# Performance work log

Hardware: AMD Instinct MI355X
Metric: run time of the kernel (lower is better)

The kernel has to match this reference:

```python
import jax, jax.numpy as jnp
import numpy as np

N_NODES = 50000
N_EDGES = 400000
N_GRAPHS = 64
DN = 64    # node features
DE = 64    # edge features
DG = 16    # global features
DH = 128   # mlp hidden
DO = 64    # mlp output
NHID = 2   # hidden layers
E_IN = 2 * DN + DE + DG   # 208
N_IN = DN + DO + DG       # 144


def _mlp_params(key, d_in, d_h, d_out, n_hid):
    ks = jax.random.split(key, 3)
    w_in = jax.random.normal(ks[0], (d_in, d_h), jnp.float32) * (2.0 / d_in) ** 0.5
    w_h = jax.random.normal(ks[1], (n_hid, d_h, d_h), jnp.float32) * (2.0 / d_h) ** 0.5
    w_out = jax.random.normal(ks[2], (d_h, d_out), jnp.float32) * (2.0 / d_h) ** 0.5
    return (w_in, jnp.zeros((d_h,), jnp.float32), w_h, jnp.zeros((n_hid, d_h), jnp.float32),
            w_out, jnp.zeros((d_out,), jnp.float32), jnp.ones((d_out,), jnp.float32),
            jnp.zeros((d_out,), jnp.float32))


def _mlp(h, w_in, b_in, w_h, b_h, w_out, b_out, g, b):
    # Lin -> [relu, Lin]*NHID -> relu -> Lin -> LayerNorm  (dropout=0 at eval)
    h = h @ w_in + b_in
    for i in range(w_h.shape[0]):
        h = jax.nn.relu(h) @ w_h[i] + b_h[i]
    h = jax.nn.relu(h) @ w_out + b_out
    mu = jnp.mean(h, axis=-1, keepdims=True)
    var = jnp.mean((h - mu) ** 2, axis=-1, keepdims=True)
    return (h - mu) * jax.lax.rsqrt(var + 1e-5) * g + b


def setup_inputs() -> dict:
    key = jax.random.key(0)
    k = jax.random.split(key, 8)
    x = jax.random.normal(k[0], (N_NODES, DN), jnp.float32)
    edge_attr = jax.random.normal(k[1], (N_EDGES, DE), jnp.float32)
    u = jax.random.normal(k[2], (N_GRAPHS, DG), jnp.float32)
    edge_index = jax.random.randint(k[3], (2, N_EDGES), 0, N_NODES, dtype=jnp.int32)
    batch = jnp.sort(jax.random.randint(k[4], (N_NODES,), 0, N_GRAPHS, dtype=jnp.int32))
    names = ["w_in", "b_in", "w_h", "b_h", "w_out", "b_out", "ln_g", "ln_b"]
    d = {"x": x, "edge_attr": edge_attr, "u": u, "edge_index": edge_index, "batch": batch}
    for pref, kk, d_in in (("e_", k[5], E_IN), ("a_", k[6], E_IN), ("n_", k[7], N_IN)):
        for nm, v in zip(names, _mlp_params(kk, d_in, DH, DO, NHID)):
            d[pref + nm] = v
    return d


def reference(x, edge_attr, u, edge_index, batch,
              e_w_in, e_b_in, e_w_h, e_b_h, e_w_out, e_b_out, e_ln_g, e_ln_b,
              a_w_in, a_b_in, a_w_h, a_b_h, a_w_out, a_b_out, a_ln_g, a_ln_b,
              n_w_in, n_b_in, n_w_h, n_b_h, n_w_out, n_b_out, n_ln_g, n_ln_b):
    src, tgt = edge_index[0], edge_index[1]
    edge_batch = batch[src]
    # EdgeModel: gather src/tgt node feats + global feats, concat, MLP (+ sigmoid attention MLP)
    neigh = jnp.concatenate([x[src], x[tgt], edge_attr, u[edge_batch]], axis=1)  # [E, E_IN]
    e_out = _mlp(neigh, e_w_in, e_b_in, e_w_h, e_b_h, e_w_out, e_b_out, e_ln_g, e_ln_b)
    attn = jax.nn.sigmoid(_mlp(neigh, a_w_in, a_b_in, a_w_h, a_b_h, a_w_out, a_b_out, a_ln_g, a_ln_b))
    e_out = e_out * attn  # [E, DO]
    # NodeModel: scatter-sum incoming (target-indexed) edge outputs, concat, MLP
    agg = jax.ops.segment_sum(e_out, tgt, num_segments=x.shape[0])  # [N, DO], zeros for isolated nodes
    node_in = jnp.concatenate([x, agg, u[batch]], axis=1)  # [N, N_IN]
    x_out = _mlp(node_in, n_w_in, n_b_in, n_w_h, n_b_h, n_w_out, n_b_out, n_ln_g, n_ln_b)
    return x_out
```

## Files before the change

kernel.cpp:

```cpp
#include <hip/hip_runtime.h>
#include <math.h>

#define N_NODES 50000
#define N_EDGES 400000

typedef _Float16 half8 __attribute__((ext_vector_type(8)));
typedef float f32x4 __attribute__((ext_vector_type(4)));

#define LD1 232
#define LDH 136
#define LDN 168

#define AGG_OFF 0
#define XH_OFF  12800000
#define UH_OFF  19200000
#define WP_OFF  19202048
#define O_EW1 0
#define O_EH0 28672
#define O_EH1 45056
#define O_EWO 61440
#define O_AW1 69632
#define O_AH0 98304
#define O_AH1 114688
#define O_AWO 131072
#define O_NW1 139264
#define O_NH0 159744
#define O_NH1 176128
#define O_NWO 192512

__device__ __forceinline__ f32x4 mfma16(half8 a, half8 b, f32x4 c) {
  return __builtin_amdgcn_mfma_f32_16x16x32_f16(a, b, c, 0, 0, 0);
}

__device__ __forceinline__ void gemm_h(const _Float16* __restrict__ src,
                                       _Float16* __restrict__ dst,
                                       const _Float16* __restrict__ wp16,
                                       const float* __restrict__ bias,
                                       int w, int lane) {
  const half8* wp = (const half8*)wp16;
  const int r = lane & 15, ch = lane >> 4;
  f32x4 a0[4], a1[4];
#pragma unroll
  for (int m = 0; m < 4; ++m) {
    a0[m] = (f32x4){0.f, 0.f, 0.f, 0.f};
    a1[m] = (f32x4){0.f, 0.f, 0.f, 0.f};
  }
#pragma unroll
  for (int s = 0; s < 4; ++s) {
    half8 b0 = wp[(s * 4 + ch) * 128 + w * 32 + r];
    half8 b1 = wp[(s * 4 + ch) * 128 + w * 32 + 16 + r];
#pragma unroll
    for (int m = 0; m < 4; ++m) {
      half8 a = *(const half8*)(src + (m * 16 + r) * LDH + s * 32 + ch * 8);
      a0[m] = mfma16(a, b0, a0[m]);
      a1[m] = mfma16(a, b1, a1[m]);
    }
  }
  float bb0 = bias[w * 32 + r], bb1 = bias[w * 32 + 16 + r];
#pragma unroll
  for (int m = 0; m < 4; ++m)
#pragma unroll
    for (int q = 0; q < 4; ++q) {
      int row = m * 16 + ch * 4 + q;
      dst[row * LDH + w * 32 + r]      = (_Float16)fmaxf(a0[m][q] + bb0, 0.f);
      dst[row * LDH + w * 32 + 16 + r] = (_Float16)fmaxf(a1[m][q] + bb1, 0.f);
    }
}

__device__ __forceinline__ void gemm_l1_dual(const _Float16* __restrict__ sIn,
                                             _Float16* __restrict__ dQ,
                                             _Float16* __restrict__ dR,
                                             const _Float16* wpE16, const _Float16* wpA16,
                                             const float* __restrict__ bE,
                                             const float* __restrict__ bA,
                                             int w, int lane) {
  const half8* wpE = (const half8*)wpE16;
  const half8* wpA = (const half8*)wpA16;
  const int r = lane & 15, ch = lane >> 4;
  f32x4 e0[4], e1[4], q0[4], q1[4];
#pragma unroll
  for (int m = 0; m < 4; ++m) {
    e0[m] = (f32x4){0.f, 0.f, 0.f, 0.f}; e1[m] = (f32x4){0.f, 0.f, 0.f, 0.f};
    q0[m] = (f32x4){0.f, 0.f, 0.f, 0.f}; q1[m] = (f32x4){0.f, 0.f, 0.f, 0.f};
  }
#pragma unroll
  for (int s = 0; s < 7; ++s) {
    half8 be0 = wpE[(s * 4 + ch) * 128 + w * 32 + r];
    half8 be1 = wpE[(s * 4 + ch) * 128 + w * 32 + 16 + r];
    half8 ba0 = wpA[(s * 4 + ch) * 128 + w * 32 + r];
    half8 ba1 = wpA[(s * 4 + ch) * 128 + w * 32 + 16 + r];
#pragma unroll
    for (int m = 0; m < 4; ++m) {
      half8 a = *(const half8*)(sIn + (m * 16 + r) * LD1 + s * 32 + ch * 8);
      e0[m] = mfma16(a, be0, e0[m]);
      e1[m] = mfma16(a, be1, e1[m]);
      q0[m] = mfma16(a, ba0, q0[m]);
      q1[m] = mfma16(a, ba1, q1[m]);
    }
  }
  float be0v = bE[w * 32 + r], be1v = bE[w * 32 + 16 + r];
  float ba0v = bA[w * 32 + r], ba1v = bA[w * 32 + 16 + r];
#pragma unroll
  for (int m = 0; m < 4; ++m)
#pragma unroll
    for (int q = 0; q < 4; ++q) {
      int row = m * 16 + ch * 4 + q;
      dQ[row * LDH + w * 32 + r]      = (_Float16)fmaxf(e0[m][q] + be0v, 0.f);
      dQ[row * LDH + w * 32 + 16 + r] = (_Float16)fmaxf(e1[m][q] + be1v, 0.f);
      dR[row * LDH + w * 32 + r]      = (_Float16)fmaxf(q0[m][q] + ba0v, 0.f);
      dR[row * LDH + w * 32 + 16 + r] = (_Float16)fmaxf(q1[m][q] + ba1v, 0.f);
    }
}

__device__ __forceinline__ void gemm_l1n(const _Float16* __restrict__ sIn,
                                         _Float16* __restrict__ dst,
                                         const _Float16* wp16,
                                         const float* __restrict__ bias,
                                         int w, int lane) {
  const half8* wp = (const half8*)wp16;
  const int r = lane & 15, ch = lane >> 4;
  f32x4 a0[4], a1[4];
#pragma unroll
  for (int m = 0; m < 4; ++m) {
    a0[m] = (f32x4){0.f, 0.f, 0.f, 0.f};
    a1[m] = (f32x4){0.f, 0.f, 0.f, 0.f};
  }
#pragma unroll
  for (int s = 0; s < 5; ++s) {
    half8 b0 = wp[(s * 4 + ch) * 128 + w * 32 + r];
    half8 b1 = wp[(s * 4 + ch) * 128 + w * 32 + 16 + r];
#pragma unroll
    for (int m = 0; m < 4; ++m) {
      half8 a = *(const half8*)(sIn + (m * 16 + r) * LDN + s * 32 + ch * 8);
      a0[m] = mfma16(a, b0, a0[m]);
      a1[m] = mfma16(a, b1, a1[m]);
    }
  }
  float bb0 = bias[w * 32 + r], bb1 = bias[w * 32 + 16 + r];
#pragma unroll
  for (int m = 0; m < 4; ++m)
#pragma unroll
    for (int q = 0; q < 4; ++q) {
      int row = m * 16 + ch * 4 + q;
      dst[row * LDH + w * 32 + r]      = (_Float16)fmaxf(a0[m][q] + bb0, 0.f);
      dst[row * LDH + w * 32 + 16 + r] = (_Float16)fmaxf(a1[m][q] + bb1, 0.f);
    }
}

struct EdgeP {
  const float* edge_attr; const int* edge_index; const int* batch;
  const _Float16* x_h; const _Float16* u_h; const _Float16* wp;
  const float *eBin, *eBh, *eBout, *eG, *eBt;
  const float *aBin, *aBh, *aBout, *aG, *aBt;
  float* agg;
};

__global__ __launch_bounds__(256, 2) void edge_kernel(EdgeP p) {
  __shared__ __align__(16) _Float16 sIn[64 * LD1];
  __shared__ __align__(16) _Float16 sQ[64 * LDH];
  __shared__ __align__(16) _Float16 sR[64 * LDH];
  __shared__ int sSrc[64], sTgt[64], sEb[64];
  const int tid = threadIdx.x;
  const int e0 = blockIdx.x * 64;

  if (tid < 64) {
    int s = p.edge_index[e0 + tid];
    sSrc[tid] = s;
    sTgt[tid] = p.edge_index[N_EDGES + e0 + tid];
    sEb[tid] = p.batch[s];
  }
  __syncthreads();

  for (int idx = tid; idx < 64 * 32; idx += 256) {
    int c = idx & 31, e = idx >> 5;
    if (c >= 29) continue;
    int col = c * 8;
    half8 v;
    if (col < 64) {
      v = *(const half8*)(p.x_h + (size_t)sSrc[e] * 64 + col);
    } else if (col < 128) {
      v = *(const half8*)(p.x_h + (size_t)sTgt[e] * 64 + col - 64);
    } else if (col < 192) {
      const float* ea = p.edge_attr + (size_t)(e0 + e) * 64 + (col - 128);
      float4 f0 = *(const float4*)ea, f1 = *(const float4*)(ea + 4);
      v[0] = (_Float16)f0.x; v[1] = (_Float16)f0.y;
      v[2] = (_Float16)f0.z; v[3] = (_Float16)f0.w;
      v[4] = (_Float16)f1.x; v[5] = (_Float16)f1.y;
      v[6] = (_Float16)f1.z; v[7] = (_Float16)f1.w;
    } else if (col < 208) {
      v = *(const half8*)(p.u_h + sEb[e] * 16 + col - 192);
    } else {
#pragma unroll
      for (int j = 0; j < 8; ++j) v[j] = (_Float16)0.f;
    }
    *(half8*)(sIn + e * LD1 + col) = v;
  }
  __syncthreads();

  const int lane = tid & 63, w = tid >> 6;
  _Float16* sP = sIn;

  gemm_l1_dual(sIn, sQ, sR, p.wp + O_EW1, p.wp + O_AW1, p.eBin, p.aBin, w, lane);
  __syncthreads();
  gemm_h(sQ, sP, p.wp + O_EH0, p.eBh, w, lane);        __syncthreads();
  gemm_h(sR, sQ, p.wp + O_AH0, p.aBh, w, lane);        __syncthreads();
  gemm_h(sP, sR, p.wp + O_EH1, p.eBh + 128, w, lane);  __syncthreads();
  gemm_h(sQ, sP, p.wp + O_AH1, p.aBh + 128, w, lane);  __syncthreads();

  const int r = lane & 15, ch = lane >> 4;
  const half8* wpEo = (const half8*)(p.wp + O_EWO);
  const half8* wpAo = (const half8*)(p.wp + O_AWO);
  f32x4 accE[4], accA[4];
#pragma unroll
  for (int t = 0; t < 4; ++t) {
    accE[t] = (f32x4){0.f, 0.f, 0.f, 0.f};
    accA[t] = (f32x4){0.f, 0.f, 0.f, 0.f};
  }
#pragma unroll
  for (int s = 0; s < 4; ++s) {
    half8 hE = *(const half8*)(sR + (w * 16 + r) * LDH + s * 32 + ch * 8);
    half8 hA = *(const half8*)(sP + (w * 16 + r) * LDH + s * 32 + ch * 8);
#pragma unroll
    for (int t = 0; t < 4; ++t) {
      half8 bEf = wpEo[(s * 4 + ch) * 64 + t * 16 + r];
      half8 bAf = wpAo[(s * 4 + ch) * 64 + t * 16 + r];
      accE[t] = mfma16(hE, bEf, accE[t]);
      accA[t] = mfma16(hA, bAf, accA[t]);
    }
  }
  float gE[4], tE[4], gA[4], tA[4];
#pragma unroll
  for (int t = 0; t < 4; ++t) {
    int cidx = t * 16 + r;
    float boE = p.eBout[cidx], boA = p.aBout[cidx];
#pragma unroll
    for (int q = 0; q < 4; ++q) { accE[t][q] += boE; accA[t][q] += boA; }
    gE[t] = p.eG[cidx]; tE[t] = p.eBt[cidx];
    gA[t] = p.aG[cidx]; tA[t] = p.aBt[cidx];
  }
#pragma unroll
  for (int q = 0; q < 4; ++q) {
    float s1e = 0.f, s2e = 0.f, s1a = 0.f, s2a = 0.f;
#pragma unroll
    for (int t = 0; t < 4; ++t) {
      float v = accE[t][q]; s1e += v; s2e += v * v;
      float u = accA[t][q]; s1a += u; s2a += u * u;
    }
#pragma unroll
    for (int mk = 1; mk < 16; mk <<= 1) {
      s1e += __shfl_xor(s1e, mk); s2e += __shfl_xor(s2e, mk);
      s1a += __shfl_xor(s1a, mk); s2a += __shfl_xor(s2a, mk);
    }
    float mue = s1e * (1.f / 64), mua = s1a * (1.f / 64);
    float rse = rsqrtf(s2e * (1.f / 64) - mue * mue + 1e-5f);
    float rsa = rsqrtf(s2a * (1.f / 64) - mua * mua + 1e-5f);
    int row = w * 16 + ch * 4 + q;
    float* ap = p.agg + (size_t)sTgt[row] * 64 + r;
#pragma unroll
    for (int t = 0; t < 4; ++t) {
      float oe = (accE[t][q] - mue) * rse * gE[t] + tE[t];
      float oa = (accA[t][q] - mua) * rsa * gA[t] + tA[t];
      atomicAdd(ap + t * 16, oe / (1.f + __expf(-oa)));
    }
  }
}

struct NodeP {
  const float* agg; const _Float16* x_h; const _Float16* u_h;
  const _Float16* wp; const int* batch;
  const float *Bin, *Bh, *Bout, *G, *Bt;
  float* out;
};

__global__ __launch_bounds__(256, 2) void node_kernel(NodeP p) {
  __shared__ __align__(16) _Float16 sIn[64 * LDN];
  __shared__ __align__(16) _Float16 sQ[64 * LDH];
  __shared__ int sB[64];
  const int tid = threadIdx.x;
  const int n0 = blockIdx.x * 64;

  if (tid < 64) {
    int n = n0 + tid;
    sB[tid] = (n < N_NODES) ? p.batch[n] : 0;
  }
  __syncthreads();

  for (int idx = tid; idx < 64 * 32; idx += 256) {
    int c = idx & 31, e = idx >> 5;
    if (c >= 21) continue;
    int n = n0 + e, col = c * 8;
    half8 v;
    if (n >= N_NODES || col >= 144) {
#pragma unroll
      for (int j = 0; j < 8; ++j) v[j] = (_Float16)0.f;
    } else if (col < 64) {
      v = *(const half8*)(p.x_h + (size_t)n * 64 + col);
    } else if (col < 128) {
      const float* ag = p.agg + (size_t)n * 64 + (col - 64);
      float4 f0 = *(const float4*)ag, f1 = *(const float4*)(ag + 4);
      v[0] = (_Float16)f0.x; v[1] = (_Float16)f0.y;
      v[2] = (_Float16)f0.z; v[3] = (_Float16)f0.w;
      v[4] = (_Float16)f1.x; v[5] = (_Float16)f1.y;
      v[6] = (_Float16)f1.z; v[7] = (_Float16)f1.w;
    } else {
      v = *(const half8*)(p.u_h + sB[e] * 16 + col - 128);
    }
    *(half8*)(sIn + e * LDN + col) = v;
  }
  __syncthreads();

  const int lane = tid & 63, w = tid >> 6;
  _Float16* sP = sIn;

  gemm_l1n(sIn, sQ, p.wp + O_NW1, p.Bin, w, lane);      __syncthreads();
  gemm_h(sQ, sP, p.wp + O_NH0, p.Bh, w, lane);          __syncthreads();
  gemm_h(sP, sQ, p.wp + O_NH1, p.Bh + 128, w, lane);    __syncthreads();

  const int r = lane & 15, ch = lane >> 4;
  const half8* wpNo = (const half8*)(p.wp + O_NWO);
  f32x4 acc[4];
#pragma unroll
  for (int t = 0; t < 4; ++t) acc[t] = (f32x4){0.f, 0.f, 0.f, 0.f};
#pragma unroll
  for (int s = 0; s < 4; ++s) {
    half8 h = *(const half8*)(sQ + (w * 16 + r) * LDH + s * 32 + ch * 8);
#pragma unroll
    for (int t = 0; t < 4; ++t) {
      half8 b = wpNo[(s * 4 + ch) * 64 + t * 16 + r];
      acc[t] = mfma16(h, b, acc[t]);
    }
  }
  float g[4], bt[4];
#pragma unroll
  for (int t = 0; t < 4; ++t) {
    int cidx = t * 16 + r;
    float bo = p.Bout[cidx];
#pragma unroll
    for (int q = 0; q < 4; ++q) acc[t][q] += bo;
    g[t] = p.G[cidx]; bt[t] = p.Bt[cidx];
  }
#pragma unroll
  for (int q = 0; q < 4; ++q) {
    float s1 = 0.f, s2 = 0.f;
#pragma unroll
    for (int t = 0; t < 4; ++t) { float v = acc[t][q]; s1 += v; s2 += v * v; }
#pragma unroll
    for (int mk = 1; mk < 16; mk <<= 1) {
      s1 += __shfl_xor(s1, mk); s2 += __shfl_xor(s2, mk);
    }
    float mu = s1 * (1.f / 64);
    float rs = rsqrtf(s2 * (1.f / 64) - mu * mu + 1e-5f);
    int row = w * 16 + ch * 4 + q;
    int n = n0 + row;
    if (n < N_NODES) {
#pragma unroll
      for (int t = 0; t < 4; ++t)
        p.out[(size_t)n * 64 + t * 16 + r] = (acc[t][q] - mu) * rs * g[t] + bt[t];
    }
  }
}

#define GX 112
struct PackP {
  const float* src[12];
  int Kreal[12], Nlog[12], size[12], dstoff[12];
  const float* x; const float* u;
  _Float16* x_h; _Float16* u_h; _Float16* wdst;
};

__global__ void pack_kernel(PackP p) {
  int y = blockIdx.y;
  int idx = blockIdx.x * 256 + threadIdx.x;
  if (y < 12) {
    int sz = p.size[y];
    if (idx >= sz) return;
    int N = 1 << p.Nlog[y];
    int j = idx & 7, t = idx >> 3;
    int n = t & (N - 1);
    int sc = t >> p.Nlog[y];
    int c = sc & 3, s = sc >> 2;
    int k = s * 32 + c * 8 + j;
    p.wdst[p.dstoff[y] + idx] =
        (k < p.Kreal[y]) ? (_Float16)p.src[y][k * N + n] : (_Float16)0.f;
  } else {
    for (int i = idx; i < N_NODES * 64; i += GX * 256) p.x_h[i] = (_Float16)p.x[i];
    for (int i = idx; i < 64 * 16; i += GX * 256) p.u_h[i] = (_Float16)p.u[i];
  }
}

extern "C" void kernel_launch(void* const* d_in, const int* in_sizes, int n_in,
                              void* d_out, int out_size, void* d_ws, size_t ws_size,
                              hipStream_t stream) {
  const float* x = (const float*)d_in[0];
  const float* edge_attr = (const float*)d_in[1];
  const float* u = (const float*)d_in[2];
  const int* edge_index = (const int*)d_in[3];
  const int* batch = (const int*)d_in[4];

  char* ws = (char*)d_ws;
  float* agg = (float*)(ws + AGG_OFF);
  _Float16* x_h = (_Float16*)(ws + XH_OFF);
  _Float16* u_h = (_Float16*)(ws + UH_OFF);
  _Float16* wp = (_Float16*)(ws + WP_OFF);

  hipMemsetAsync(agg, 0, (size_t)N_NODES * 64 * sizeof(float), stream);

  PackP pk;
  const float* eWh = (const float*)d_in[7];
  const float* aWh = (const float*)d_in[15];
  const float* nWh = (const float*)d_in[23];
  const float* srcs[12] = {
      (const float*)d_in[5], eWh, eWh + 16384, (const float*)d_in[9],
      (const float*)d_in[13], aWh, aWh + 16384, (const float*)d_in[17],
      (const float*)d_in[21], nWh, nWh + 16384, (const float*)d_in[25]};
  const int kr[12] = {208, 128, 128, 128, 208, 128, 128, 128, 144, 128, 128, 128};
  const int nl[12] = {7, 7, 7, 6, 7, 7, 7, 6, 7, 7, 7, 6};
  const int sz[12] = {28672, 16384, 16384, 8192, 28672, 16384, 16384, 8192,
                      20480, 16384, 16384, 8192};
  const int off[12] = {O_EW1, O_EH0, O_EH1, O_EWO, O_AW1, O_AH0, O_AH1, O_AWO,
                       O_NW1, O_NH0, O_NH1, O_NWO};
  for (int i = 0; i < 12; ++i) {
    pk.src[i] = srcs[i]; pk.Kreal[i] = kr[i]; pk.Nlog[i] = nl[i];
    pk.size[i] = sz[i]; pk.dstoff[i] = off[i];
  }
  pk.x = x; pk.u = u; pk.x_h = x_h; pk.u_h = u_h; pk.wdst = wp;
  pack_kernel<<<dim3(GX, 13), 256, 0, stream>>>(pk);

  EdgeP ep;
  ep.edge_attr = edge_attr; ep.edge_index = edge_index; ep.batch = batch;
  ep.x_h = x_h; ep.u_h = u_h; ep.wp = wp;
  ep.eBin = (const float*)d_in[6];  ep.eBh = (const float*)d_in[8];
  ep.eBout = (const float*)d_in[10]; ep.eG = (const float*)d_in[11];
  ep.eBt = (const float*)d_in[12];
  ep.aBin = (const float*)d_in[14]; ep.aBh = (const float*)d_in[16];
  ep.aBout = (const float*)d_in[18]; ep.aG = (const float*)d_in[19];
  ep.aBt = (const float*)d_in[20];
  ep.agg = agg;
  edge_kernel<<<N_EDGES / 64, 256, 0, stream>>>(ep);

  NodeP np;
  np.agg = agg; np.x_h = x_h; np.u_h = u_h; np.wp = wp; np.batch = batch;
  np.Bin = (const float*)d_in[22]; np.Bh = (const float*)d_in[24];
  np.Bout = (const float*)d_in[26]; np.G = (const float*)d_in[27];
  np.Bt = (const float*)d_in[28];
  np.out = (float*)d_out;
  node_kernel<<<(N_NODES + 63) / 64, 256, 0, stream>>>(np);
}
```

Baseline: 594.4 us.

## Split edge and attention MLPs across separate wave groups in 512-thread blocks

The edge kernel now runs 512 threads: waves 0-3 compute the edge MLP and waves 4-7 compute the attention MLP concurrently, each with its own ping-pong LDS buffers, instead of four waves computing both MLPs serially. The attention waves write sigmoid values to shared memory and the edge waves combine them before the scatter-add atomics. Index staging in shared memory is removed; each thread reads edge_index and batch directly, and the zero-padding column of the input tile is no longer written. This halves the per-wave serial GEMM chain and raises parallelism, at the cost of more LDS per block (four buffers) and an extra barrier; launch bounds of 512 threads with 4 blocks per CU may restrict registers.

```diff
diff --git a/kernel.cpp b/kernel.cpp
--- a/kernel.cpp
+++ b/kernel.cpp
@@ -32,7 +32,8 @@
   return __builtin_amdgcn_mfma_f32_16x16x32_f16(a, b, c, 0, 0, 0);
 }
 
-__device__ __forceinline__ void gemm_h(const _Float16* __restrict__ src,
+template<int NS, int LDSRC>
+__device__ __forceinline__ void gemm32(const _Float16* __restrict__ src,
                                        _Float16* __restrict__ dst,
                                        const _Float16* __restrict__ wp16,
                                        const float* __restrict__ bias,
@@ -46,92 +47,12 @@
     a1[m] = (f32x4){0.f, 0.f, 0.f, 0.f};
   }
 #pragma unroll
-  for (int s = 0; s < 4; ++s) {
+  for (int s = 0; s < NS; ++s) {
     half8 b0 = wp[(s * 4 + ch) * 128 + w * 32 + r];
     half8 b1 = wp[(s * 4 + ch) * 128 + w * 32 + 16 + r];
 #pragma unroll
     for (int m = 0; m < 4; ++m) {
-      half8 a = *(const half8*)(src + (m * 16 + r) * LDH + s * 32 + ch * 8);
-      a0[m] = mfma16(a, b0, a0[m]);
-      a1[m] = mfma16(a, b1, a1[m]);
-    }
-  }
-  float bb0 = bias[w * 32 + r], bb1 = bias[w * 32 + 16 + r];
-#pragma unroll
-  for (int m = 0; m < 4; ++m)
-#pragma unroll
-    for (int q = 0; q < 4; ++q) {
-      int row = m * 16 + ch * 4 + q;
-      dst[row * LDH + w * 32 + r]      = (_Float16)fmaxf(a0[m][q] + bb0, 0.f);
-      dst[row * LDH + w * 32 + 16 + r] = (_Float16)fmaxf(a1[m][q] + bb1, 0.f);
-    }
-}
-
-__device__ __forceinline__ void gemm_l1_dual(const _Float16* __restrict__ sIn,
-                                             _Float16* __restrict__ dQ,
-                                             _Float16* __restrict__ dR,
-                                             const _Float16* wpE16, const _Float16* wpA16,
-                                             const float* __restrict__ bE,
-                                             const float* __restrict__ bA,
-                                             int w, int lane) {
-  const half8* wpE = (const half8*)wpE16;
-  const half8* wpA = (const half8*)wpA16;
-  const int r = lane & 15, ch = lane >> 4;
-  f32x4 e0[4], e1[4], q0[4], q1[4];
-#pragma unroll
-  for (int m = 0; m < 4; ++m) {
-    e0[m] = (f32x4){0.f, 0.f, 0.f, 0.f}; e1[m] = (f32x4){0.f, 0.f, 0.f, 0.f};
-    q0[m] = (f32x4){0.f, 0.f, 0.f, 0.f}; q1[m] = (f32x4){0.f, 0.f, 0.f, 0.f};
-  }
-#pragma unroll
-  for (int s = 0; s < 7; ++s) {
-    half8 be0 = wpE[(s * 4 + ch) * 128 + w * 32 + r];
-    half8 be1 = wpE[(s * 4 + ch) * 128 + w * 32 + 16 + r];
-    half8 ba0 = wpA[(s * 4 + ch) * 128 + w * 32 + r];
-    half8 ba1 = wpA[(s * 4 + ch) * 128 + w * 32 + 16 + r];
-#pragma unroll
-    for (int m = 0; m < 4; ++m) {
-      half8 a = *(const half8*)(sIn + (m * 16 + r) * LD1 + s * 32 + ch * 8);
-      e0[m] = mfma16(a, be0, e0[m]);
-      e1[m] = mfma16(a, be1, e1[m]);
-      q0[m] = mfma16(a, ba0, q0[m]);
-      q1[m] = mfma16(a, ba1, q1[m]);
-    }
-  }
-  float be0v = bE[w * 32 + r], be1v = bE[w * 32 + 16 + r];
-  float ba0v = bA[w * 32 + r], ba1v = bA[w * 32 + 16 + r];
-#pragma unroll
-  for (int m = 0; m < 4; ++m)
-#pragma unroll
-    for (int q = 0; q < 4; ++q) {
-      int row = m * 16 + ch * 4 + q;
-      dQ[row * LDH + w * 32 + r]      = (_Float16)fmaxf(e0[m][q] + be0v, 0.f);
-      dQ[row * LDH + w * 32 + 16 + r] = (_Float16)fmaxf(e1[m][q] + be1v, 0.f);
-      dR[row * LDH + w * 32 + r]      = (_Float16)fmaxf(q0[m][q] + ba0v, 0.f);
-      dR[row * LDH + w * 32 + 16 + r] = (_Float16)fmaxf(q1[m][q] + ba1v, 0.f);
-    }
-}
-
-__device__ __forceinline__ void gemm_l1n(const _Float16* __restrict__ sIn,
-                                         _Float16* __restrict__ dst,
-                                         const _Float16* wp16,
-                                         const float* __restrict__ bias,
-                                         int w, int lane) {
-  const half8* wp = (const half8*)wp16;
-  const int r = lane & 15, ch = lane >> 4;
-  f32x4 a0[4], a1[4];
-#pragma unroll
-  for (int m = 0; m < 4; ++m) {
-    a0[m] = (f32x4){0.f, 0.f, 0.f, 0.f};
-    a1[m] = (f32x4){0.f, 0.f, 0.f, 0.f};
-  }
-#pragma unroll
-  for (int s = 0; s < 5; ++s) {
-    half8 b0 = wp[(s * 4 + ch) * 128 + w * 32 + r];
-    half8 b1 = wp[(s * 4 + ch) * 128 + w * 32 + 16 + r];
-#pragma unroll
-    for (int m = 0; m < 4; ++m) {
-      half8 a = *(const half8*)(sIn + (m * 16 + r) * LDN + s * 32 + ch * 8);
+      half8 a = *(const half8*)(src + (m * 16 + r) * LDSRC + s * 32 + ch * 8);
       a0[m] = mfma16(a, b0, a0[m]);
       a1[m] = mfma16(a, b1, a1[m]);
     }
@@ -155,31 +76,25 @@
   float* agg;
 };
 
-__global__ __launch_bounds__(256, 2) void edge_kernel(EdgeP p) {
+__global__ __launch_bounds__(512, 4) void edge_kernel(EdgeP p) {
   __shared__ __align__(16) _Float16 sIn[64 * LD1];
-  __shared__ __align__(16) _Float16 sQ[64 * LDH];
-  __shared__ __align__(16) _Float16 sR[64 * LDH];
-  __shared__ int sSrc[64], sTgt[64], sEb[64];
+  __shared__ __align__(16) _Float16 sQe[64 * LDH];
+  __shared__ __align__(16) _Float16 sQa[64 * LDH];
+  __shared__ __align__(16) _Float16 sPa[64 * LDH];
   const int tid = threadIdx.x;
   const int e0 = blockIdx.x * 64;
 
-  if (tid < 64) {
-    int s = p.edge_index[e0 + tid];
-    sSrc[tid] = s;
-    sTgt[tid] = p.edge_index[N_EDGES + e0 + tid];
-    sEb[tid] = p.batch[s];
-  }
-  __syncthreads();
-
-  for (int idx = tid; idx < 64 * 32; idx += 256) {
+  for (int idx = tid; idx < 64 * 32; idx += 512) {
     int c = idx & 31, e = idx >> 5;
-    if (c >= 29) continue;
+    if (c >= 28) continue;
     int col = c * 8;
     half8 v;
     if (col < 64) {
-      v = *(const half8*)(p.x_h + (size_t)sSrc[e] * 64 + col);
+      int s = p.edge_index[e0 + e];
+      v = *(const half8*)(p.x_h + (size_t)s * 64 + col);
     } else if (col < 128) {
-      v = *(const half8*)(p.x_h + (size_t)sTgt[e] * 64 + col - 64);
+      int t = p.edge_index[N_EDGES + e0 + e];
+      v = *(const half8*)(p.x_h + (size_t)t * 64 + col - 64);
     } else if (col < 192) {
       const float* ea = p.edge_attr + (size_t)(e0 + e) * 64 + (col - 128);
       float4 f0 = *(const float4*)ea, f1 = *(const float4*)(ea + 4);
@@ -188,7 +103,9 @@
       v[4] = (_Float16)f1.x; v[5] = (_Float16)f1.y;
       v[6] = (_Float16)f1.z; v[7] = (_Float16)f1.w;
     } else if (col < 208) {
-      v = *(const half8*)(p.u_h + sEb[e] * 16 + col - 192);
+      int s = p.edge_index[e0 + e];
+      int eb = p.batch[s];
+      v = *(const half8*)(p.u_h + eb * 16 + col - 192);
     } else {
 #pragma unroll
       for (int j = 0; j < 8; ++j) v[j] = (_Float16)0.f;
@@ -197,70 +114,82 @@
   }
   __syncthreads();
 
-  const int lane = tid & 63, w = tid >> 6;
-  _Float16* sP = sIn;
-
-  gemm_l1_dual(sIn, sQ, sR, p.wp + O_EW1, p.wp + O_AW1, p.eBin, p.aBin, w, lane);
-  __syncthreads();
-  gemm_h(sQ, sP, p.wp + O_EH0, p.eBh, w, lane);        __syncthreads();
-  gemm_h(sR, sQ, p.wp + O_AH0, p.aBh, w, lane);        __syncthreads();
-  gemm_h(sP, sR, p.wp + O_EH1, p.eBh + 128, w, lane);  __syncthreads();
-  gemm_h(sQ, sP, p.wp + O_AH1, p.aBh + 128, w, lane);  __syncthreads();
+  const int lane = tid & 63, wid = tid >> 6, we = wid & 3;
+  const bool isE = wid < 4;
+  _Float16* ping = isE ? sQe : sQa;
+  _Float16* pong = isE ? sIn : sPa;
+  const _Float16* w1 = p.wp + (isE ? O_EW1 : O_AW1);
+  const _Float16* h0 = p.wp + (isE ? O_EH0 : O_AH0);
+  const _Float16* h1 = p.wp + (isE ? O_EH1 : O_AH1);
+  const _Float16* wo = p.wp + (isE ? O_EWO : O_AWO);
+  const float* bin = isE ? p.eBin : p.aBin;
+  const float* bh  = isE ? p.eBh  : p.aBh;
+  const float* bo  = isE ? p.eBout: p.aBout;
+  const float* g   = isE ? p.eG   : p.aG;
+  const float* bt  = isE ? p.eBt  : p.aBt;
+
+  gemm32<7, LD1>(sIn,  ping, w1, bin,      we, lane); __syncthreads();
+  gemm32<4, LDH>(ping, pong, h0, bh,       we, lane); __syncthreads();
+  gemm32<4, LDH>(pong, ping, h1, bh + 128, we, lane); __syncthreads();
 
   const int r = lane & 15, ch = lane >> 4;
-  const half8* wpEo = (const half8*)(p.wp + O_EWO);
-  const half8* wpAo = (const half8*)(p.wp + O_AWO);
-  f32x4 accE[4], accA[4];
-#pragma unroll
-  for (int t = 0; t < 4; ++t) {
-    accE[t] = (f32x4){0.f, 0.f, 0.f, 0.f};
-    accA[t] = (f32x4){0.f, 0.f, 0.f, 0.f};
-  }
+  const half8* wpo = (const half8*)wo;
+  f32x4 acc[4];
+#pragma unroll
+  for (int t = 0; t < 4; ++t) acc[t] = (f32x4){0.f, 0.f, 0.f, 0.f};
 #pragma unroll
   for (int s = 0; s < 4; ++s) {
-    half8 hE = *(const half8*)(sR + (w * 16 + r) * LDH + s * 32 + ch * 8);
-    half8 hA = *(const half8*)(sP + (w * 16 + r) * LDH + s * 32 + ch * 8);
-#pragma unroll
-    for (int t = 0; t < 4; ++t) {
-      half8 bEf = wpEo[(s * 4 + ch) * 64 + t * 16 + r];
-      half8 bAf = wpAo[(s * 4 + ch) * 64 + t * 16 + r];
-      accE[t] = mfma16(hE, bEf, accE[t]);
-      accA[t] = mfma16(hA, bAf, accA[t]);
-    }
-  }
-  float gE[4], tE[4], gA[4], tA[4];
+    half8 a = *(const half8*)(ping + (we * 16 + r) * LDH + s * 32 + ch * 8);
+#pragma unroll
+    for (int t = 0; t < 4; ++t)
+      acc[t] = mfma16(a, wpo[(s * 4 + ch) * 64 + t * 16 + r], acc[t]);
+  }
+  float gg[4], tt[4];
 #pragma unroll
   for (int t = 0; t < 4; ++t) {
     int cidx = t * 16 + r;
-    float boE = p.eBout[cidx], boA = p.aBout[cidx];
-#pragma unroll
-    for (int q = 0; q < 4; ++q) { accE[t][q] += boE; accA[t][q] += boA; }
-    gE[t] = p.eG[cidx]; tE[t] = p.eBt[cidx];
-    gA[t] = p.aG[cidx]; tA[t] = p.aBt[cidx];
-  }
+    float bov = bo[cidx];
+#pragma unroll
+    for (int q = 0; q < 4; ++q) acc[t][q] += bov;
+    gg[t] = g[cidx]; tt[t] = bt[cidx];
+  }
+  float mu_[4], rs_[4];
 #pragma unroll
   for (int q = 0; q < 4; ++q) {
-    float s1e = 0.f, s2e = 0.f, s1a = 0.f, s2a = 0.f;
-#pragma unroll
-    for (int t = 0; t < 4; ++t) {
-      float v = accE[t][q]; s1e += v; s2e += v * v;
-      float u = accA[t][q]; s1a += u; s2a += u * u;
-    }
+    float s1 = 0.f, s2 = 0.f;
+#pragma unroll
+    for (int t = 0; t < 4; ++t) { float v = acc[t][q]; s1 += v; s2 += v * v; }
 #pragma unroll
     for (int mk = 1; mk < 16; mk <<= 1) {
-      s1e += __shfl_xor(s1e, mk); s2e += __shfl_xor(s2e, mk);
-      s1a += __shfl_xor(s1a, mk); s2a += __shfl_xor(s2a, mk);
-    }
-    float mue = s1e * (1.f / 64), mua = s1a * (1.f / 64);
-    float rse = rsqrtf(s2e * (1.f / 64) - mue * mue + 1e-5f);
-    float rsa = rsqrtf(s2a * (1.f / 64) - mua * mua + 1e-5f);
-    int row = w * 16 + ch * 4 + q;
-    float* ap = p.agg + (size_t)sTgt[row] * 64 + r;
-#pragma unroll
-    for (int t = 0; t < 4; ++t) {
-      float oe = (accE[t][q] - mue) * rse * gE[t] + tE[t];
-      float oa = (accA[t][q] - mua) * rsa * gA[t] + tA[t];
-      atomicAdd(ap + t * 16, oe / (1.f + __expf(-oa)));
+      s1 += __shfl_xor(s1, mk); s2 += __shfl_xor(s2, mk);
+    }
+    mu_[q] = s1 * (1.f / 64);
+    rs_[q] = rsqrtf(s2 * (1.f / 64) - mu_[q] * mu_[q] + 1e-5f);
+  }
+  float* cmb = (float*)sPa;
+  if (!isE) {
+#pragma unroll
+    for (int q = 0; q < 4; ++q) {
+      int row = we * 16 + ch * 4 + q;
+#pragma unroll
+      for (int t = 0; t < 4; ++t) {
+        float oa = (acc[t][q] - mu_[q]) * rs_[q] * gg[t] + tt[t];
+        cmb[row * 64 + t * 16 + r] = 1.f / (1.f + __expf(-oa));
+      }
+    }
+  }
+  __syncthreads();
+  if (isE) {
+#pragma unroll
+    for (int q = 0; q < 4; ++q) {
+      int row = we * 16 + ch * 4 + q;
+      int tgt = p.edge_index[N_EDGES + e0 + row];
+      float* ap = p.agg + (size_t)tgt * 64 + r;
+#pragma unroll
+      for (int t = 0; t < 4; ++t) {
+        float oe = (acc[t][q] - mu_[q]) * rs_[q] * gg[t] + tt[t];
+        atomicAdd(ap + t * 16, oe * cmb[row * 64 + t * 16 + r]);
+      }
     }
   }
 }
@@ -312,9 +241,9 @@
   const int lane = tid & 63, w = tid >> 6;
   _Float16* sP = sIn;
 
-  gemm_l1n(sIn, sQ, p.wp + O_NW1, p.Bin, w, lane);      __syncthreads();
-  gemm_h(sQ, sP, p.wp + O_NH0, p.Bh, w, lane);          __syncthreads();
-  gemm_h(sP, sQ, p.wp + O_NH1, p.Bh + 128, w, lane);    __syncthreads();
+  gemm32<5, LDN>(sIn, sQ, p.wp + O_NW1, p.Bin, w, lane);      __syncthreads();
+  gemm32<4, LDH>(sQ, sP, p.wp + O_NH0, p.Bh, w, lane);        __syncthreads();
+  gemm32<4, LDH>(sP, sQ, p.wp + O_NH1, p.Bh + 128, w, lane);  __syncthreads();
 
   const int r = lane & 15, ch = lane >> 4;
   const half8* wpNo = (const half8*)(p.wp + O_NWO);
@@ -334,9 +263,9 @@
 #pragma unroll
   for (int t = 0; t < 4; ++t) {
     int cidx = t * 16 + r;
-    float bo = p.Bout[cidx];
-#pragma unroll
-    for (int q = 0; q < 4; ++q) acc[t][q] += bo;
+    float bov = p.Bout[cidx];
+#pragma unroll
+    for (int q = 0; q < 4; ++q) acc[t][q] += bov;
     g[t] = p.G[cidx]; bt[t] = p.Bt[cidx];
   }
 #pragma unroll
@@ -436,7 +365,7 @@
   ep.aBout = (const float*)d_in[18]; ep.aG = (const float*)d_in[19];
   ep.aBt = (const float*)d_in[20];
   ep.agg = agg;
-  edge_kernel<<<N_EDGES / 64, 256, 0, stream>>>(ep);
+  edge_kernel<<<N_EDGES / 64, 512, 0, stream>>>(ep);
 
   NodeP np;
   np.agg = agg; np.x_h = x_h; np.u_h = u_h; np.wp = wp; np.batch = batch;
```

After: 551.3 us. -7.3%, faster.
